# Optimization experiments

Hardware: AMD Instinct MI355X
Metric: run time of the kernel (lower is better)

## Reference

```python
import jax, jax.numpy as jnp
import numpy as np

C_REG = 0.1
MAX_ITER = 15
SIGMA = 0.1  # centering parameter for the interior-point steps


def _qp_solve(G, e, h, A, b, max_iter):
    """Batched primal-dual interior-point solver (fixed iteration count, as QPFunction(maxIter=...)).

    Solves per task: min_z 0.5 z^T G z + e^T z  s.t.  z <= h (inequality matrix is identity),  A z = b.
    G: (t,n,n), e,h: (t,n), A: (t,p,n), b: (t,p). Returns z: (t,n).
    """
    t, n = e.shape
    p = A.shape[1]
    dt = G.dtype
    z = jnp.zeros((t, n), dt)
    s = jnp.ones((t, n), dt)    # slack for z + s = h
    lam = jnp.ones((t, n), dt)  # inequality duals
    nu = jnp.zeros((t, p), dt)  # equality duals
    At = jnp.swapaxes(A, 1, 2)              # (t,n,p)
    eye_n = jnp.eye(n, dtype=dt)
    zeros_pp = jnp.zeros((t, p, p), dt)

    def step(carry, _):
        z, s, lam, nu = carry
        # KKT residuals (infeasible-start Newton)
        rz = jnp.einsum('bij,bj->bi', G, z) + e + lam + jnp.einsum('bpi,bp->bi', A, nu)
        rs = z + s - h
        ra = jnp.einsum('bpi,bi->bp', A, z) - b
        mu = jnp.mean(lam * s, axis=1, keepdims=True)
        # eliminate ds and dlam -> reduced saddle system in (dz, dnu)
        r1 = -rz - (lam * rs - lam * s + SIGMA * mu) / s
        D = lam / s  # diagonal of barrier Hessian contribution
        M_top = jnp.concatenate([G + D[:, :, None] * eye_n, At], axis=2)  # (t,n,n+p)
        M_bot = jnp.concatenate([A, zeros_pp], axis=2)                    # (t,p,n+p)
        M = jnp.concatenate([M_top, M_bot], axis=1)                       # (t,n+p,n+p)
        rhs = jnp.concatenate([r1, -ra], axis=1)
        sol = jnp.linalg.solve(M, rhs[..., None])[..., 0]
        dz, dnu = sol[:, :n], sol[:, n:]
        ds = -rs - dz
        dlam = (lam * dz + lam * rs - lam * s + SIGMA * mu) / s
        # fraction-to-boundary step size keeping s, lam > 0
        ratio_s = jnp.where(ds < 0, -s / ds, jnp.inf)
        ratio_l = jnp.where(dlam < 0, -lam / dlam, jnp.inf)
        alpha = jnp.minimum(1.0, 0.99 * jnp.minimum(ratio_s.min(axis=1), ratio_l.min(axis=1)))[:, None]
        return (z + alpha * dz, s + alpha * ds, lam + alpha * dlam, nu + alpha * dnu), None

    (z, s, lam, nu), _ = jax.lax.scan(step, (z, s, lam, nu), xs=None, length=max_iter)
    return z


def setup_inputs() -> dict:
    key = jax.random.key(0)
    k1, k2, k3 = jax.random.split(key, 3)
    tasks, n_way, n_shot, d = 64, 5, 15, 4096
    n_support = n_way * n_shot          # 75
    n_query = 150
    query = jax.random.normal(k1, (tasks, n_query, d), dtype=jnp.float32)
    support = jax.random.normal(k2, (tasks, n_support, d), dtype=jnp.float32)
    support_labels = jax.random.randint(k3, (tasks, n_support), 0, n_way)
    return {"query": query, "support": support, "support_labels": support_labels,
            "n_way": n_way, "n_shot": n_shot}


def reference(query, support, support_labels, n_way, n_shot):
    t, ns, d = support.shape
    nq = query.shape[1]
    n = ns * n_way
    dt = support.dtype
    # linear kernel Gram matrix on support: (t, ns, ns)
    K = jnp.einsum('bnd,bmd->bnm', support, support)
    # block kernel = K kron I_{n_way}, then + I (the module adds 1.0 * eye)
    I_w = jnp.eye(n_way, dtype=dt)
    block_K = (K[:, :, None, :, None] * I_w[None, None, :, None, :]).reshape(t, n, n)
    G = block_K + jnp.eye(n, dtype=dt)
    # one-hot labels, flattened to (t, ns*n_way)
    y1h = jax.nn.one_hot(support_labels, n_way, dtype=dt).reshape(t, n)
    e = -y1h
    h = C_REG * y1h
    # A = I_{ns} kron ones(1, n_way): sums duals over classes per support point
    A = jnp.tile(jnp.eye(ns, dtype=dt)[:, :, None], (1, 1, n_way)).reshape(ns, n)
    A = jnp.broadcast_to(A, (t, ns, n))
    b = jnp.zeros((t, ns), dt)
    z = _qp_solve(G, e, h, A, b, MAX_ITER)
    qp_sol = z.reshape(t, ns, n_way)
    # compatibility = support . query^T : (t, ns, nq); logits = sum over support
    compat = jnp.einsum('bnd,bqd->bnq', support, query)
    logits = jnp.einsum('bnq,bnw->bqw', compat, qp_sol)  # (t, nq, n_way)
    return logits
```

## Files before the change

kernel.cpp:

```cpp
#include <hip/hip_runtime.h>
#include <math.h>

#define T_TASKS 64
#define NS 75
#define NW 5
#define NTOT 375
#define NQ 150
#define DIM 4096
#define QP_ITERS 15
#define SIGMA 0.1f
#define CREG 0.1f

#define OFF_K   0u
#define OFF_W   369664u
#define OFF_Z   2417664u
#define OFF_S   2441664u
#define OFF_LAM 2465664u
#define OFF_NU  2489664u
#define OFF_TV  2494464u

__global__ void qp_init(float* __restrict__ z, float* __restrict__ s,
                        float* __restrict__ lam, float* __restrict__ nu) {
    int idx = blockIdx.x * 256 + threadIdx.x;
    if (idx < T_TASKS * NTOT) { z[idx] = 0.f; s[idx] = 1.f; lam[idx] = 1.f; }
    if (idx < T_TASKS * NS) nu[idx] = 0.f;
}

__global__ __launch_bounds__(256) void gram_partial(const float* __restrict__ support,
                                                    float* __restrict__ Kp) {
    int qd = blockIdx.x, b = blockIdx.y;
    __shared__ __align__(16) float Ss[80 * 132];
    int tid = threadIdx.x;
    int tx = tid & 15, ty = tid >> 4;
    float acc[5][5];
#pragma unroll
    for (int u = 0; u < 5; u++)
#pragma unroll
        for (int v = 0; v < 5; v++) acc[u][v] = 0.f;
    const float* sb = support + (size_t)b * NS * DIM + qd * 1024;
    for (int cc = 0; cc < 8; cc++) {
        __syncthreads();
        for (int idx = tid; idx < 80 * 32; idx += 256) {
            int r = idx >> 5, d4 = idx & 31;
            float4 v = make_float4(0.f, 0.f, 0.f, 0.f);
            if (r < 75) v = *(const float4*)&sb[(size_t)r * DIM + cc * 128 + d4 * 4];
            *(float4*)&Ss[r * 132 + d4 * 4] = v;
        }
        __syncthreads();
        for (int d4 = 0; d4 < 32; d4++) {
            float4 av[5], bv[5];
#pragma unroll
            for (int u = 0; u < 5; u++) av[u] = *(const float4*)&Ss[(ty * 5 + u) * 132 + d4 * 4];
#pragma unroll
            for (int v = 0; v < 5; v++) bv[v] = *(const float4*)&Ss[(tx * 5 + v) * 132 + d4 * 4];
#pragma unroll
            for (int u = 0; u < 5; u++)
#pragma unroll
                for (int v = 0; v < 5; v++)
                    acc[u][v] += av[u].x * bv[v].x + av[u].y * bv[v].y +
                                 av[u].z * bv[v].z + av[u].w * bv[v].w;
        }
    }
    float* Ko = Kp + (size_t)(qd * 64 + b) * 5776;
#pragma unroll
    for (int u = 0; u < 5; u++) {
        int row = ty * 5 + u;
#pragma unroll
        for (int v = 0; v < 5; v++) {
            int col = tx * 5 + v;
            if (row < 75 && col < 75) Ko[row * 76 + col] = acc[u][v];
        }
    }
}

__global__ void gram_reduce(const float* __restrict__ Kp, float* __restrict__ Kg) {
    int idx = blockIdx.x * 256 + threadIdx.x;
    if (idx >= 64 * 5776) return;
    int rc = idx % 5776;
    int row = rc / 76, col = rc % 76;
    float val;
    if (row < 75 && col < 75)
        val = Kp[idx] + Kp[369664 + idx] + Kp[2 * 369664 + idx] + Kp[3 * 369664 + idx];
    else
        val = (row == col) ? 1.f : 0.f;
    Kg[idx] = val;
}

__device__ __forceinline__ void reg_gj80(float (&M)[5][5],
                                         float (*prow)[80], float (*fcol)[80],
                                         int tx, int ty) {
    for (int k = 0; k < 75; k++) {
        int bf = k & 1;
        if (ty == (k & 15)) {
#pragma unroll
            for (int m = 0; m < 5; m++) {
                if (ty + 16 * m == k) {
#pragma unroll
                    for (int n = 0; n < 5; n++) prow[bf][tx + 16 * n] = M[m][n];
                }
            }
        }
        if (tx == (k & 15)) {
#pragma unroll
            for (int n = 0; n < 5; n++) {
                if (tx + 16 * n == k) {
#pragma unroll
                    for (int m = 0; m < 5; m++) fcol[bf][ty + 16 * m] = M[m][n];
                }
            }
        }
        __syncthreads();
        float pinv = 1.f / prow[bf][k];
        float pv[5], fv[5], ps[5];
#pragma unroll
        for (int n = 0; n < 5; n++) {
            pv[n] = prow[bf][tx + 16 * n];
            ps[n] = pv[n] * pinv;
        }
#pragma unroll
        for (int m = 0; m < 5; m++) {
            int r = ty + 16 * m;
            float f = fcol[bf][r] * pinv;
            fv[m] = (r == k) ? 0.f : f;
        }
#pragma unroll
        for (int m = 0; m < 5; m++) {
            int r = ty + 16 * m;
            bool rk = (r == k);
#pragma unroll
            for (int n = 0; n < 5; n++) {
                int c = tx + 16 * n;
                float val = M[m][n] - fv[m] * pv[n];
                val = rk ? ps[n] : val;
                val = (c == k) ? (rk ? pinv : -fv[m]) : val;
                M[m][n] = val;
            }
        }
    }
}

__global__ __launch_bounds__(256) void factor_kernel(
        const float* __restrict__ Kg, const int* __restrict__ labels,
        const float* __restrict__ zg, const float* __restrict__ sg,
        const float* __restrict__ lamg, const float* __restrict__ nug,
        float* __restrict__ Wg, float* __restrict__ tvg) {
    int w = blockIdx.x, b = blockIdx.y;
    int tid = threadIdx.x;
    int tx = tid & 15, ty = tid >> 4;
    __shared__ float prow[2][80], fcol[2][80];
    __shared__ float zw[80], r1w[80], Dv[80], swv[80], lwv[80], nuwv[80];
    __shared__ int labv[80];
    __shared__ float mred[4];

    float M[5][5];
    const float* Kt = Kg + (size_t)b * 5776;
#pragma unroll
    for (int m = 0; m < 5; m++) {
        int r = ty + 16 * m;
#pragma unroll
        for (int n = 0; n < 5; n++) {
            int c = tx + 16 * n;
            M[m][n] = (r < 76 && c < 76) ? Kt[r * 76 + c] : ((r == c) ? 1.f : 0.f);
        }
    }
    if (tid < 80) {
        float zv = 0.f, sv = 1.f, lv = 0.f, nv = 0.f; int lb = -1;
        if (tid < 75) {
            zv = zg[b * NTOT + tid * NW + w];
            sv = sg[b * NTOT + tid * NW + w];
            lv = lamg[b * NTOT + tid * NW + w];
            nv = nug[b * NS + tid];
            lb = labels[b * NS + tid];
        }
        zw[tid] = zv; swv[tid] = sv; lwv[tid] = lv; nuwv[tid] = nv; labv[tid] = lb;
    }
    float part = 0.f;
    for (int idx = tid; idx < NTOT; idx += 256)
        part += lamg[b * NTOT + idx] * sg[b * NTOT + idx];
#pragma unroll
    for (int off = 32; off > 0; off >>= 1) part += __shfl_xor(part, off, 64);
    if ((tid & 63) == 0) mred[tid >> 6] = part;
    __syncthreads();
    float mu = (mred[0] + mred[1] + mred[2] + mred[3]) * (1.f / (float)NTOT);

    float gp[5];
#pragma unroll
    for (int m = 0; m < 5; m++) {
        float a = 0.f;
#pragma unroll
        for (int n = 0; n < 5; n++) a += M[m][n] * zw[tx + 16 * n];
        gp[m] = a;
    }
#pragma unroll
    for (int off = 1; off < 16; off <<= 1)
#pragma unroll
        for (int m = 0; m < 5; m++) gp[m] += __shfl_xor(gp[m], off, 64);
    if (tx == 0) {
#pragma unroll
        for (int m = 0; m < 5; m++) {
            int r = ty + 16 * m;
            float val = 0.f, dv = 0.f;
            if (r < 75) {
                float sv = swv[r], lv = lwv[r], zv = zw[r];
                float e = (labv[r] == w) ? -1.f : 0.f;
                float h = (labv[r] == w) ? CREG : 0.f;
                float rz = gp[m] + zv + e + lv + nuwv[r];
                float rs = zv + sv - h;
                val = -rz - (lv * rs - lv * sv + SIGMA * mu) / sv;
                dv = lv / sv;
            }
            r1w[r] = val; Dv[r] = dv;
        }
    }
    __syncthreads();
    if (tx == ty) {
#pragma unroll
        for (int m = 0; m < 5; m++) {
            int r = ty + 16 * m;
            if (r < 75) M[m][m] += 1.f + Dv[r];
        }
    }

    reg_gj80(M, prow, fcol, tx, ty);

    float* Wo = Wg + (size_t)(b * NW + w) * 6400;
#pragma unroll
    for (int m = 0; m < 5; m++)
#pragma unroll
        for (int n = 0; n < 5; n++)
            Wo[(m * 5 + n) * 256 + tid] = M[m][n];

    float tp[5];
#pragma unroll
    for (int m = 0; m < 5; m++) {
        float a = 0.f;
#pragma unroll
        for (int n = 0; n < 5; n++) a += M[m][n] * r1w[tx + 16 * n];
        tp[m] = a;
    }
#pragma unroll
    for (int off = 1; off < 16; off <<= 1)
#pragma unroll
        for (int m = 0; m < 5; m++) tp[m] += __shfl_xor(tp[m], off, 64);
    if (tx == 0) {
#pragma unroll
        for (int m = 0; m < 5; m++) {
            int r = ty + 16 * m;
            if (r < 75) tvg[(b * NW + w) * 80 + r] = tp[m];
        }
    }
}

__global__ __launch_bounds__(256) void schur_update_kernel(
        const int* __restrict__ labels,
        float* __restrict__ z, float* __restrict__ s,
        float* __restrict__ lam, float* __restrict__ nu,
        const float* __restrict__ Wg, const float* __restrict__ tvg) {
    int b = blockIdx.x;
    int tid = threadIdx.x;
    int tx = tid & 15, ty = tid >> 4;
    __shared__ float prow[2][80], fcol[2][80];
    __shared__ __align__(16) float rhs[80];
    __shared__ __align__(16) float dnu[80];
    __shared__ float mred[4], ared[4];

    float M[5][5];
    const float* Wb = Wg + (size_t)b * NW * 6400;
#pragma unroll
    for (int m = 0; m < 5; m++)
#pragma unroll
        for (int n = 0; n < 5; n++) {
            float a = 0.f;
#pragma unroll
            for (int ww = 0; ww < 5; ww++)
                a += Wb[ww * 6400 + (m * 5 + n) * 256 + tid];
            M[m][n] = a;
        }
    if (tid < 80) {
        float rv = 0.f;
        if (tid < 75) {
#pragma unroll
            for (int ww = 0; ww < 5; ww++)
                rv += z[b * NTOT + tid * NW + ww] + tvg[(b * NW + ww) * 80 + tid];
        }
        rhs[tid] = rv;
    }
    float part = 0.f;
    for (int idx = tid; idx < NTOT; idx += 256)
        part += lam[b * NTOT + idx] * s[b * NTOT + idx];
#pragma unroll
    for (int off = 32; off > 0; off >>= 1) part += __shfl_xor(part, off, 64);
    if ((tid & 63) == 0) mred[tid >> 6] = part;
    __syncthreads();
    float mu = (mred[0] + mred[1] + mred[2] + mred[3]) * (1.f / (float)NTOT);

    reg_gj80(M, prow, fcol, tx, ty);

    float tp[5];
#pragma unroll
    for (int m = 0; m < 5; m++) {
        float a = 0.f;
#pragma unroll
        for (int n = 0; n < 5; n++) a += M[m][n] * rhs[tx + 16 * n];
        tp[m] = a;
    }
#pragma unroll
    for (int off = 1; off < 16; off <<= 1)
#pragma unroll
        for (int m = 0; m < 5; m++) tp[m] += __shfl_xor(tp[m], off, 64);
    if (tx == 0) {
#pragma unroll
        for (int m = 0; m < 5; m++) dnu[ty + 16 * m] = tp[m];
    }
    __syncthreads();

    float rat = INFINITY;
    float dzv[2], dsv[2], dlv[2], zlv[2], slv[2], llv[2];
#pragma unroll
    for (int pass = 0; pass < 2; pass++) {
        int c = tid + 256 * pass;
        dzv[pass] = 0.f; dsv[pass] = 0.f; dlv[pass] = 0.f;
        zlv[pass] = 0.f; slv[pass] = 1.f; llv[pass] = 0.f;
        if (c < NTOT) {
            int i = c / 5, ww = c - (c / 5) * 5;
            int mi = i >> 4, tyi = i & 15;
            const float* Wr = Wb + ww * 6400 + mi * 5 * 256 + tyi * 16;
            const float4* dn4 = (const float4*)dnu;
            float acc = 0.f;
#pragma unroll
            for (int n = 0; n < 5; n++) {
                const float4* w4 = (const float4*)(Wr + n * 256);
#pragma unroll
                for (int q = 0; q < 4; q++) {
                    float4 x = w4[q], y = dn4[4 * n + q];
                    acc += x.x * y.x + x.y * y.y + x.z * y.z + x.w * y.w;
                }
            }
            float tvl = tvg[(b * NW + ww) * 80 + i];
            float zl = z[b * NTOT + c], sl = s[b * NTOT + c], ll = lam[b * NTOT + c];
            float dz_t = tvl - acc;
            int lb = labels[b * NS + i];
            float h = (lb == ww) ? CREG : 0.f;
            float rs = zl + sl - h;
            float ds_t = -rs - dz_t;
            float dl_t = (ll * dz_t + ll * rs - ll * sl + SIGMA * mu) / sl;
            zlv[pass] = zl; slv[pass] = sl; llv[pass] = ll;
            dzv[pass] = dz_t; dsv[pass] = ds_t; dlv[pass] = dl_t;
            float r1 = (ds_t < 0.f) ? (-sl / ds_t) : INFINITY;
            float r2 = (dl_t < 0.f) ? (-ll / dl_t) : INFINITY;
            rat = fminf(rat, fminf(r1, r2));
        }
    }
#pragma unroll
    for (int off = 32; off > 0; off >>= 1) rat = fminf(rat, __shfl_xor(rat, off, 64));
    if ((tid & 63) == 0) ared[tid >> 6] = rat;
    __syncthreads();
    float alpha = fminf(1.f, 0.99f * fminf(fminf(ared[0], ared[1]), fminf(ared[2], ared[3])));
#pragma unroll
    for (int pass = 0; pass < 2; pass++) {
        int c = tid + 256 * pass;
        if (c < NTOT) {
            z[b * NTOT + c]   = zlv[pass] + alpha * dzv[pass];
            s[b * NTOT + c]   = slv[pass] + alpha * dsv[pass];
            lam[b * NTOT + c] = llv[pass] + alpha * dlv[pass];
        }
    }
    if (tid < 75) nu[b * NS + tid] += alpha * dnu[tid];
}

__global__ __launch_bounds__(256) void v_kernel(const float* __restrict__ support,
                                                const float* __restrict__ z,
                                                float* __restrict__ vbuf) {
    int dc = blockIdx.x, b = blockIdx.y;
    __shared__ float zs[NTOT];
    int tid = threadIdx.x;
    for (int idx = tid; idx < NTOT; idx += 256) zs[idx] = z[b * NTOT + idx];
    __syncthreads();
    int d = dc * 256 + tid;
    float acc[5] = {0.f, 0.f, 0.f, 0.f, 0.f};
    const float* sb = support + (size_t)b * NS * DIM + d;
    for (int ss = 0; ss < NS; ss++) {
        float svv = sb[(size_t)ss * DIM];
#pragma unroll
        for (int w = 0; w < 5; w++) acc[w] += svv * zs[ss * 5 + w];
    }
#pragma unroll
    for (int w = 0; w < 5; w++) vbuf[(size_t)(b * NW + w) * DIM + d] = acc[w];
}

__global__ __launch_bounds__(256) void logits_kernel(const float* __restrict__ query,
                                                     const float* __restrict__ vbuf,
                                                     float* __restrict__ out) {
    int qt = blockIdx.x, b = blockIdx.y;
    __shared__ __align__(16) float vs[5 * 1028];
    int tid = threadIdx.x;
    int lane = tid & 63, wid = tid >> 6;
    float acc[8][5];
#pragma unroll
    for (int r = 0; r < 8; r++)
#pragma unroll
        for (int w = 0; w < 5; w++) acc[r][w] = 0.f;

    for (int c = 0; c < 4; c++) {
        __syncthreads();
        for (int idx = tid; idx < 5120; idx += 256) {
            int w = idx >> 10, dd = idx & 1023;
            vs[w * 1028 + dd] = vbuf[(size_t)(b * NW + w) * DIM + c * 1024 + dd];
        }
        __syncthreads();
#pragma unroll
        for (int ri = 0; ri < 8; ri++) {
            int r = wid + ri * 4;
            if (r < 30) {
                int q = qt * 30 + r;
                const float* qp = query + (size_t)(b * NQ + q) * DIM + c * 1024;
#pragma unroll
                for (int j = 0; j < 4; j++) {
                    int d = lane * 4 + j * 256;
                    float4 qv = *(const float4*)(qp + d);
#pragma unroll
                    for (int w = 0; w < 5; w++) {
                        float4 vv = *(const float4*)(&vs[w * 1028 + d]);
                        acc[ri][w] += qv.x * vv.x + qv.y * vv.y + qv.z * vv.z + qv.w * vv.w;
                    }
                }
            }
        }
    }
#pragma unroll
    for (int ri = 0; ri < 8; ri++) {
        int r = wid + ri * 4;
#pragma unroll
        for (int w = 0; w < 5; w++) {
            float v = acc[ri][w];
            for (int off = 32; off > 0; off >>= 1) v += __shfl_xor(v, off, 64);
            if (r < 30 && lane == 0)
                out[(size_t)(b * NQ + qt * 30 + r) * NW + w] = v;
        }
    }
}

extern "C" void kernel_launch(void* const* d_in, const int* in_sizes, int n_in,
                              void* d_out, int out_size, void* d_ws, size_t ws_size,
                              hipStream_t stream) {
    const float* query   = (const float*)d_in[0];
    const float* support = (const float*)d_in[1];
    const int*   labels  = (const int*)d_in[2];
    float* out = (float*)d_out;
    float* ws  = (float*)d_ws;

    float* Kg   = ws + OFF_K;
    float* Wg   = ws + OFF_W;
    float* Kp   = ws + OFF_W;
    float* vbuf = ws + OFF_W;
    float* z    = ws + OFF_Z;
    float* s    = ws + OFF_S;
    float* lam  = ws + OFF_LAM;
    float* nu   = ws + OFF_NU;
    float* tv   = ws + OFF_TV;

    qp_init<<<(T_TASKS * NTOT + 255) / 256, 256, 0, stream>>>(z, s, lam, nu);
    gram_partial<<<dim3(4, T_TASKS), 256, 0, stream>>>(support, Kp);
    gram_reduce<<<(64 * 5776 + 255) / 256, 256, 0, stream>>>(Kp, Kg);
    for (int it = 0; it < QP_ITERS; it++) {
        factor_kernel<<<dim3(NW, T_TASKS), 256, 0, stream>>>(Kg, labels, z, s, lam, nu, Wg, tv);
        schur_update_kernel<<<T_TASKS, 256, 0, stream>>>(labels, z, s, lam, nu, Wg, tv);
    }
    v_kernel<<<dim3(16, T_TASKS), 256, 0, stream>>>(support, z, vbuf);
    logits_kernel<<<dim3(5, T_TASKS), 256, 0, stream>>>(query, vbuf, out);
}
```

Before: 2.167 ms.

## Fuse all QP iterations into one persistent per-task kernel with register-resident inverses

Replaces the 30 per-iteration launches (factor and Schur update) with a single kernel per task that keeps z, s, lambda and nu in shared memory and holds all five class-block inverses in registers across all 15 iterations. This removes global round-trips of the W matrices and the launch overhead. The Gram kernel is also split 8 ways with double-buffered prefetch and stores only the lower triangle. In exchange, only 64 blocks run during the QP phase and register pressure is high (launch_bounds 256,1), so occupancy and possible spilling are the risks.

```diff
diff --git a/kernel.cpp b/kernel.cpp
--- a/kernel.cpp
+++ b/kernel.cpp
@@ -14,22 +14,12 @@
 #define OFF_K   0u
 #define OFF_W   369664u
 #define OFF_Z   2417664u
-#define OFF_S   2441664u
-#define OFF_LAM 2465664u
-#define OFF_NU  2489664u
-#define OFF_TV  2494464u
-
-__global__ void qp_init(float* __restrict__ z, float* __restrict__ s,
-                        float* __restrict__ lam, float* __restrict__ nu) {
-    int idx = blockIdx.x * 256 + threadIdx.x;
-    if (idx < T_TASKS * NTOT) { z[idx] = 0.f; s[idx] = 1.f; lam[idx] = 1.f; }
-    if (idx < T_TASKS * NS) nu[idx] = 0.f;
-}
-
-__global__ __launch_bounds__(256) void gram_partial(const float* __restrict__ support,
-                                                    float* __restrict__ Kp) {
-    int qd = blockIdx.x, b = blockIdx.y;
-    __shared__ __align__(16) float Ss[80 * 132];
+#define TRI_SZ  2850
+
+__global__ __launch_bounds__(256) void gram8(const float* __restrict__ support,
+                                             float* __restrict__ Kp) {
+    int p = blockIdx.x, b = blockIdx.y;
+    __shared__ __align__(16) float Ss[2][80][68];
     int tid = threadIdx.x;
     int tx = tid & 15, ty = tid >> 4;
     float acc[5][5];
@@ -37,22 +27,39 @@
     for (int u = 0; u < 5; u++)
 #pragma unroll
         for (int v = 0; v < 5; v++) acc[u][v] = 0.f;
-    const float* sb = support + (size_t)b * NS * DIM + qd * 1024;
-    for (int cc = 0; cc < 8; cc++) {
-        __syncthreads();
-        for (int idx = tid; idx < 80 * 32; idx += 256) {
-            int r = idx >> 5, d4 = idx & 31;
-            float4 v = make_float4(0.f, 0.f, 0.f, 0.f);
-            if (r < 75) v = *(const float4*)&sb[(size_t)r * DIM + cc * 128 + d4 * 4];
-            *(float4*)&Ss[r * 132 + d4 * 4] = v;
-        }
-        __syncthreads();
-        for (int d4 = 0; d4 < 32; d4++) {
+    const float* sb = support + (size_t)b * NS * DIM + p * 512;
+
+    float4 pf[5];
+#define G8_ISSUE(c)                                                        \
+    {                                                                      \
+        _Pragma("unroll")                                                  \
+        for (int j = 0; j < 5; j++) {                                      \
+            int idx = tid + 256 * j;                                       \
+            int r = idx >> 4, q = idx & 15;                                \
+            pf[j] = (r < 75) ? *(const float4*)&sb[(size_t)r * DIM + (c) * 64 + q * 4] \
+                             : make_float4(0.f, 0.f, 0.f, 0.f);            \
+        }                                                                  \
+    }
+#define G8_COMMIT(c)                                                       \
+    {                                                                      \
+        _Pragma("unroll")                                                  \
+        for (int j = 0; j < 5; j++) {                                      \
+            int idx = tid + 256 * j;                                       \
+            int r = idx >> 4, q = idx & 15;                                \
+            *(float4*)&Ss[(c) & 1][r][q * 4] = pf[j];                      \
+        }                                                                  \
+    }
+    G8_ISSUE(0);
+    G8_COMMIT(0);
+    for (int c = 0; c < 8; c++) {
+        if (c < 7) G8_ISSUE(c + 1);
+        __syncthreads();
+        for (int d4 = 0; d4 < 16; d4++) {
             float4 av[5], bv[5];
 #pragma unroll
-            for (int u = 0; u < 5; u++) av[u] = *(const float4*)&Ss[(ty * 5 + u) * 132 + d4 * 4];
-#pragma unroll
-            for (int v = 0; v < 5; v++) bv[v] = *(const float4*)&Ss[(tx * 5 + v) * 132 + d4 * 4];
+            for (int u = 0; u < 5; u++) av[u] = *(const float4*)&Ss[c & 1][ty * 5 + u][d4 * 4];
+#pragma unroll
+            for (int v = 0; v < 5; v++) bv[v] = *(const float4*)&Ss[c & 1][tx * 5 + v][d4 * 4];
 #pragma unroll
             for (int u = 0; u < 5; u++)
 #pragma unroll
@@ -60,329 +67,355 @@
                     acc[u][v] += av[u].x * bv[v].x + av[u].y * bv[v].y +
                                  av[u].z * bv[v].z + av[u].w * bv[v].w;
         }
-    }
-    float* Ko = Kp + (size_t)(qd * 64 + b) * 5776;
+        if (c < 7) G8_COMMIT(c + 1);
+    }
+    float* Ko = Kp + (size_t)(p * 64 + b) * TRI_SZ;
 #pragma unroll
     for (int u = 0; u < 5; u++) {
         int row = ty * 5 + u;
 #pragma unroll
         for (int v = 0; v < 5; v++) {
             int col = tx * 5 + v;
-            if (row < 75 && col < 75) Ko[row * 76 + col] = acc[u][v];
+            if (row < 75 && col < 75 && row >= col)
+                Ko[row * (row + 1) / 2 + col] = acc[u][v];
         }
     }
 }
 
 __global__ void gram_reduce(const float* __restrict__ Kp, float* __restrict__ Kg) {
     int idx = blockIdx.x * 256 + threadIdx.x;
-    if (idx >= 64 * 5776) return;
-    int rc = idx % 5776;
+    if (idx >= T_TASKS * 5776) return;
+    int b = idx / 5776, rc = idx % 5776;
     int row = rc / 76, col = rc % 76;
     float val;
-    if (row < 75 && col < 75)
-        val = Kp[idx] + Kp[369664 + idx] + Kp[2 * 369664 + idx] + Kp[3 * 369664 + idx];
-    else
+    if (row < 75 && col < 75) {
+        int i = row > col ? row : col, j = row > col ? col : row;
+        int t = i * (i + 1) / 2 + j;
+        val = 0.f;
+#pragma unroll
+        for (int p = 0; p < 8; p++)
+            val += Kp[(size_t)(p * 64 + b) * TRI_SZ + t];
+    } else {
         val = (row == col) ? 1.f : 0.f;
+    }
     Kg[idx] = val;
 }
 
-__device__ __forceinline__ void reg_gj80(float (&M)[5][5],
-                                         float (*prow)[80], float (*fcol)[80],
-                                         int tx, int ty) {
+template <int NM>
+__device__ __forceinline__ void reg_gj_multi(float (&M)[NM][5][5],
+                                             float (*prow)[2][80],
+                                             float (*fcol)[2][80],
+                                             int tx, int ty) {
     for (int k = 0; k < 75; k++) {
         int bf = k & 1;
-        if (ty == (k & 15)) {
-#pragma unroll
-            for (int m = 0; m < 5; m++) {
+        int km = k & 15, kd = k >> 4;
+        if (ty == km) {
+#pragma unroll
+            for (int m = 0; m < 5; m++)
                 if (ty + 16 * m == k) {
 #pragma unroll
-                    for (int n = 0; n < 5; n++) prow[bf][tx + 16 * n] = M[m][n];
-                }
-            }
-        }
-        if (tx == (k & 15)) {
-#pragma unroll
-            for (int n = 0; n < 5; n++) {
+                    for (int w = 0; w < NM; w++)
+#pragma unroll
+                        for (int n = 0; n < 5; n++)
+                            prow[w][bf][tx + 16 * n] = M[w][m][n];
+                }
+        }
+        if (tx == km) {
+#pragma unroll
+            for (int n = 0; n < 5; n++)
                 if (tx + 16 * n == k) {
 #pragma unroll
-                    for (int m = 0; m < 5; m++) fcol[bf][ty + 16 * m] = M[m][n];
-                }
-            }
-        }
-        __syncthreads();
-        float pinv = 1.f / prow[bf][k];
-        float pv[5], fv[5], ps[5];
-#pragma unroll
-        for (int n = 0; n < 5; n++) {
-            pv[n] = prow[bf][tx + 16 * n];
-            ps[n] = pv[n] * pinv;
-        }
-#pragma unroll
-        for (int m = 0; m < 5; m++) {
-            int r = ty + 16 * m;
-            float f = fcol[bf][r] * pinv;
-            fv[m] = (r == k) ? 0.f : f;
-        }
-#pragma unroll
-        for (int m = 0; m < 5; m++) {
-            int r = ty + 16 * m;
-            bool rk = (r == k);
+                    for (int w = 0; w < NM; w++)
+#pragma unroll
+                        for (int m = 0; m < 5; m++)
+                            fcol[w][bf][ty + 16 * m] = M[w][m][n];
+                }
+        }
+        __syncthreads();
+        if (tx == km) {
+#pragma unroll
+            for (int n = 0; n < 5; n++)
+                if (n == kd) {
+#pragma unroll
+                    for (int w = 0; w < NM; w++)
+#pragma unroll
+                        for (int m = 0; m < 5; m++)
+                            M[w][m][n] = (ty + 16 * m == k) ? 1.f : 0.f;
+                }
+        }
+#pragma unroll
+        for (int w = 0; w < NM; w++) {
+            float pinv = 1.f / prow[w][bf][k];
+            float pv2[5], fv2[5];
 #pragma unroll
             for (int n = 0; n < 5; n++) {
                 int c = tx + 16 * n;
-                float val = M[m][n] - fv[m] * pv[n];
-                val = rk ? ps[n] : val;
-                val = (c == k) ? (rk ? pinv : -fv[m]) : val;
-                M[m][n] = val;
-            }
-        }
-    }
-}
-
-__global__ __launch_bounds__(256) void factor_kernel(
+                float pp = prow[w][bf][c];
+                pv2[n] = (c == k) ? 1.f : pp;
+            }
+#pragma unroll
+            for (int m = 0; m < 5; m++) {
+                int r = ty + 16 * m;
+                float f = fcol[w][bf][r] * pinv;
+                fv2[m] = (r == k) ? (1.f - pinv) : f;
+            }
+#pragma unroll
+            for (int m = 0; m < 5; m++)
+#pragma unroll
+                for (int n = 0; n < 5; n++)
+                    M[w][m][n] -= fv2[m] * pv2[n];
+        }
+    }
+}
+
+__global__ __launch_bounds__(256, 1) void qp_solve(
         const float* __restrict__ Kg, const int* __restrict__ labels,
-        const float* __restrict__ zg, const float* __restrict__ sg,
-        const float* __restrict__ lamg, const float* __restrict__ nug,
-        float* __restrict__ Wg, float* __restrict__ tvg) {
-    int w = blockIdx.x, b = blockIdx.y;
-    int tid = threadIdx.x;
-    int tx = tid & 15, ty = tid >> 4;
-    __shared__ float prow[2][80], fcol[2][80];
-    __shared__ float zw[80], r1w[80], Dv[80], swv[80], lwv[80], nuwv[80];
-    __shared__ int labv[80];
-    __shared__ float mred[4];
-
-    float M[5][5];
-    const float* Kt = Kg + (size_t)b * 5776;
-#pragma unroll
-    for (int m = 0; m < 5; m++) {
-        int r = ty + 16 * m;
-#pragma unroll
-        for (int n = 0; n < 5; n++) {
-            int c = tx + 16 * n;
-            M[m][n] = (r < 76 && c < 76) ? Kt[r * 76 + c] : ((r == c) ? 1.f : 0.f);
-        }
-    }
-    if (tid < 80) {
-        float zv = 0.f, sv = 1.f, lv = 0.f, nv = 0.f; int lb = -1;
-        if (tid < 75) {
-            zv = zg[b * NTOT + tid * NW + w];
-            sv = sg[b * NTOT + tid * NW + w];
-            lv = lamg[b * NTOT + tid * NW + w];
-            nv = nug[b * NS + tid];
-            lb = labels[b * NS + tid];
-        }
-        zw[tid] = zv; swv[tid] = sv; lwv[tid] = lv; nuwv[tid] = nv; labv[tid] = lb;
-    }
-    float part = 0.f;
-    for (int idx = tid; idx < NTOT; idx += 256)
-        part += lamg[b * NTOT + idx] * sg[b * NTOT + idx];
-#pragma unroll
-    for (int off = 32; off > 0; off >>= 1) part += __shfl_xor(part, off, 64);
-    if ((tid & 63) == 0) mred[tid >> 6] = part;
-    __syncthreads();
-    float mu = (mred[0] + mred[1] + mred[2] + mred[3]) * (1.f / (float)NTOT);
-
-    float gp[5];
-#pragma unroll
-    for (int m = 0; m < 5; m++) {
-        float a = 0.f;
-#pragma unroll
-        for (int n = 0; n < 5; n++) a += M[m][n] * zw[tx + 16 * n];
-        gp[m] = a;
-    }
-#pragma unroll
-    for (int off = 1; off < 16; off <<= 1)
-#pragma unroll
-        for (int m = 0; m < 5; m++) gp[m] += __shfl_xor(gp[m], off, 64);
-    if (tx == 0) {
-#pragma unroll
-        for (int m = 0; m < 5; m++) {
-            int r = ty + 16 * m;
-            float val = 0.f, dv = 0.f;
-            if (r < 75) {
-                float sv = swv[r], lv = lwv[r], zv = zw[r];
-                float e = (labv[r] == w) ? -1.f : 0.f;
-                float h = (labv[r] == w) ? CREG : 0.f;
-                float rz = gp[m] + zv + e + lv + nuwv[r];
-                float rs = zv + sv - h;
-                val = -rz - (lv * rs - lv * sv + SIGMA * mu) / sv;
-                dv = lv / sv;
-            }
-            r1w[r] = val; Dv[r] = dv;
-        }
-    }
-    __syncthreads();
-    if (tx == ty) {
-#pragma unroll
-        for (int m = 0; m < 5; m++) {
-            int r = ty + 16 * m;
-            if (r < 75) M[m][m] += 1.f + Dv[r];
-        }
-    }
-
-    reg_gj80(M, prow, fcol, tx, ty);
-
-    float* Wo = Wg + (size_t)(b * NW + w) * 6400;
-#pragma unroll
-    for (int m = 0; m < 5; m++)
-#pragma unroll
-        for (int n = 0; n < 5; n++)
-            Wo[(m * 5 + n) * 256 + tid] = M[m][n];
-
-    float tp[5];
-#pragma unroll
-    for (int m = 0; m < 5; m++) {
-        float a = 0.f;
-#pragma unroll
-        for (int n = 0; n < 5; n++) a += M[m][n] * r1w[tx + 16 * n];
-        tp[m] = a;
-    }
-#pragma unroll
-    for (int off = 1; off < 16; off <<= 1)
-#pragma unroll
-        for (int m = 0; m < 5; m++) tp[m] += __shfl_xor(tp[m], off, 64);
-    if (tx == 0) {
-#pragma unroll
-        for (int m = 0; m < 5; m++) {
-            int r = ty + 16 * m;
-            if (r < 75) tvg[(b * NW + w) * 80 + r] = tp[m];
-        }
-    }
-}
-
-__global__ __launch_bounds__(256) void schur_update_kernel(
-        const int* __restrict__ labels,
-        float* __restrict__ z, float* __restrict__ s,
-        float* __restrict__ lam, float* __restrict__ nu,
-        const float* __restrict__ Wg, const float* __restrict__ tvg) {
+        float* __restrict__ zout) {
     int b = blockIdx.x;
     int tid = threadIdx.x;
     int tx = tid & 15, ty = tid >> 4;
-    __shared__ float prow[2][80], fcol[2][80];
-    __shared__ __align__(16) float rhs[80];
-    __shared__ __align__(16) float dnu[80];
-    __shared__ float mred[4], ared[4];
-
-    float M[5][5];
-    const float* Wb = Wg + (size_t)b * NW * 6400;
-#pragma unroll
-    for (int m = 0; m < 5; m++)
+
+    __shared__ float prow[5][2][80], fcol[5][2][80];
+    __shared__ float zs[400], ss[400], ls[400];
+    __shared__ float nus[80];
+    __shared__ int labv[80];
+    __shared__ float r1w[5][80], Dv[5][80], tvs[5][80], dzs[5][80];
+    __shared__ float rhs[80], dnu[80], mred[4], ared[4];
+
+    float Kreg[5][5];
+    const float* Kt = Kg + (size_t)b * 5776;
+#pragma unroll
+    for (int m = 0; m < 5; m++) {
+        int r = ty + 16 * m;
 #pragma unroll
         for (int n = 0; n < 5; n++) {
-            float a = 0.f;
-#pragma unroll
-            for (int ww = 0; ww < 5; ww++)
-                a += Wb[ww * 6400 + (m * 5 + n) * 256 + tid];
-            M[m][n] = a;
-        }
+            int c = tx + 16 * n;
+            Kreg[m][n] = (r < 76 && c < 76) ? Kt[r * 76 + c] : ((r == c) ? 1.f : 0.f);
+        }
+    }
+    for (int idx = tid; idx < 400; idx += 256) {
+        zs[idx] = 0.f;
+        ss[idx] = (idx < NTOT) ? 1.f : 0.f;
+        ls[idx] = (idx < NTOT) ? 1.f : 0.f;
+    }
     if (tid < 80) {
-        float rv = 0.f;
-        if (tid < 75) {
-#pragma unroll
-            for (int ww = 0; ww < 5; ww++)
-                rv += z[b * NTOT + tid * NW + ww] + tvg[(b * NW + ww) * 80 + tid];
-        }
-        rhs[tid] = rv;
-    }
-    float part = 0.f;
-    for (int idx = tid; idx < NTOT; idx += 256)
-        part += lam[b * NTOT + idx] * s[b * NTOT + idx];
-#pragma unroll
-    for (int off = 32; off > 0; off >>= 1) part += __shfl_xor(part, off, 64);
-    if ((tid & 63) == 0) mred[tid >> 6] = part;
+        nus[tid] = 0.f;
+        labv[tid] = (tid < 75) ? labels[b * NS + tid] : -1;
+    }
     __syncthreads();
-    float mu = (mred[0] + mred[1] + mred[2] + mred[3]) * (1.f / (float)NTOT);
-
-    reg_gj80(M, prow, fcol, tx, ty);
-
-    float tp[5];
-#pragma unroll
-    for (int m = 0; m < 5; m++) {
-        float a = 0.f;
-#pragma unroll
-        for (int n = 0; n < 5; n++) a += M[m][n] * rhs[tx + 16 * n];
-        tp[m] = a;
-    }
-#pragma unroll
-    for (int off = 1; off < 16; off <<= 1)
-#pragma unroll
-        for (int m = 0; m < 5; m++) tp[m] += __shfl_xor(tp[m], off, 64);
-    if (tx == 0) {
-#pragma unroll
-        for (int m = 0; m < 5; m++) dnu[ty + 16 * m] = tp[m];
-    }
-    __syncthreads();
-
-    float rat = INFINITY;
-    float dzv[2], dsv[2], dlv[2], zlv[2], slv[2], llv[2];
-#pragma unroll
-    for (int pass = 0; pass < 2; pass++) {
-        int c = tid + 256 * pass;
-        dzv[pass] = 0.f; dsv[pass] = 0.f; dlv[pass] = 0.f;
-        zlv[pass] = 0.f; slv[pass] = 1.f; llv[pass] = 0.f;
-        if (c < NTOT) {
-            int i = c / 5, ww = c - (c / 5) * 5;
-            int mi = i >> 4, tyi = i & 15;
-            const float* Wr = Wb + ww * 6400 + mi * 5 * 256 + tyi * 16;
-            const float4* dn4 = (const float4*)dnu;
-            float acc = 0.f;
+
+    float MW[5][5][5];
+    float S[1][5][5];
+
+    for (int it = 0; it < QP_ITERS; it++) {
+        {
+            float part = 0.f;
+            for (int idx = tid; idx < NTOT; idx += 256) part += ls[idx] * ss[idx];
+#pragma unroll
+            for (int off = 32; off > 0; off >>= 1) part += __shfl_xor(part, off, 64);
+            if ((tid & 63) == 0) mred[tid >> 6] = part;
+        }
+        __syncthreads();
+        float mu = (mred[0] + mred[1] + mred[2] + mred[3]) * (1.f / (float)NTOT);
+
+#pragma unroll
+        for (int w = 0; w < 5; w++) {
+            float gp[5];
+#pragma unroll
+            for (int m = 0; m < 5; m++) {
+                float a = 0.f;
+#pragma unroll
+                for (int n = 0; n < 5; n++) a += Kreg[m][n] * zs[(tx + 16 * n) * 5 + w];
+                gp[m] = a;
+            }
+#pragma unroll
+            for (int off = 1; off < 16; off <<= 1)
+#pragma unroll
+                for (int m = 0; m < 5; m++) gp[m] += __shfl_xor(gp[m], off, 64);
+            if (tx == 0) {
+#pragma unroll
+                for (int m = 0; m < 5; m++) {
+                    int r = ty + 16 * m;
+                    float val = 0.f, dv = 0.f;
+                    if (r < 75) {
+                        float sv = ss[r * 5 + w], lv = ls[r * 5 + w], zv = zs[r * 5 + w];
+                        float e = (labv[r] == w) ? -1.f : 0.f;
+                        float h = (labv[r] == w) ? CREG : 0.f;
+                        float rz = gp[m] + zv + e + lv + nus[r];
+                        float rs = zv + sv - h;
+                        val = -rz - (lv * rs - lv * sv + SIGMA * mu) / sv;
+                        dv = lv / sv;
+                    }
+                    r1w[w][r] = val;
+                    Dv[w][r] = dv;
+                }
+            }
+        }
+        __syncthreads();
+
+#pragma unroll
+        for (int w = 0; w < 5; w++) {
+            float dval[5];
+#pragma unroll
+            for (int m = 0; m < 5; m++) dval[m] = Dv[w][ty + 16 * m];
+#pragma unroll
+            for (int m = 0; m < 5; m++) {
+                int r = ty + 16 * m;
+#pragma unroll
+                for (int n = 0; n < 5; n++) {
+                    float v = Kreg[m][n];
+                    if (m == n && tx == ty && r < 75) v += 1.f + dval[m];
+                    MW[w][m][n] = v;
+                }
+            }
+        }
+
+        reg_gj_multi<5>(MW, prow, fcol, tx, ty);
+
+#pragma unroll
+        for (int w = 0; w < 5; w++) {
+            float tp[5];
+#pragma unroll
+            for (int m = 0; m < 5; m++) {
+                float a = 0.f;
+#pragma unroll
+                for (int n = 0; n < 5; n++) a += MW[w][m][n] * r1w[w][tx + 16 * n];
+                tp[m] = a;
+            }
+#pragma unroll
+            for (int off = 1; off < 16; off <<= 1)
+#pragma unroll
+                for (int m = 0; m < 5; m++) tp[m] += __shfl_xor(tp[m], off, 64);
+            if (tx == 0) {
+#pragma unroll
+                for (int m = 0; m < 5; m++) tvs[w][ty + 16 * m] = tp[m];
+            }
+        }
+        __syncthreads();
+
+#pragma unroll
+        for (int m = 0; m < 5; m++)
 #pragma unroll
             for (int n = 0; n < 5; n++) {
-                const float4* w4 = (const float4*)(Wr + n * 256);
-#pragma unroll
-                for (int q = 0; q < 4; q++) {
-                    float4 x = w4[q], y = dn4[4 * n + q];
-                    acc += x.x * y.x + x.y * y.y + x.z * y.z + x.w * y.w;
-                }
-            }
-            float tvl = tvg[(b * NW + ww) * 80 + i];
-            float zl = z[b * NTOT + c], sl = s[b * NTOT + c], ll = lam[b * NTOT + c];
-            float dz_t = tvl - acc;
-            int lb = labels[b * NS + i];
-            float h = (lb == ww) ? CREG : 0.f;
-            float rs = zl + sl - h;
-            float ds_t = -rs - dz_t;
-            float dl_t = (ll * dz_t + ll * rs - ll * sl + SIGMA * mu) / sl;
-            zlv[pass] = zl; slv[pass] = sl; llv[pass] = ll;
-            dzv[pass] = dz_t; dsv[pass] = ds_t; dlv[pass] = dl_t;
-            float r1 = (ds_t < 0.f) ? (-sl / ds_t) : INFINITY;
-            float r2 = (dl_t < 0.f) ? (-ll / dl_t) : INFINITY;
-            rat = fminf(rat, fminf(r1, r2));
-        }
-    }
-#pragma unroll
-    for (int off = 32; off > 0; off >>= 1) rat = fminf(rat, __shfl_xor(rat, off, 64));
-    if ((tid & 63) == 0) ared[tid >> 6] = rat;
-    __syncthreads();
-    float alpha = fminf(1.f, 0.99f * fminf(fminf(ared[0], ared[1]), fminf(ared[2], ared[3])));
-#pragma unroll
-    for (int pass = 0; pass < 2; pass++) {
-        int c = tid + 256 * pass;
-        if (c < NTOT) {
-            z[b * NTOT + c]   = zlv[pass] + alpha * dzv[pass];
-            s[b * NTOT + c]   = slv[pass] + alpha * dsv[pass];
-            lam[b * NTOT + c] = llv[pass] + alpha * dlv[pass];
-        }
-    }
-    if (tid < 75) nu[b * NS + tid] += alpha * dnu[tid];
+                float a = MW[0][m][n];
+#pragma unroll
+                for (int w = 1; w < 5; w++) a += MW[w][m][n];
+                S[0][m][n] = a;
+            }
+        if (tid < 80) {
+            float rv = 0.f;
+            if (tid < 75) {
+#pragma unroll
+                for (int w = 0; w < 5; w++) rv += zs[tid * 5 + w] + tvs[w][tid];
+            }
+            rhs[tid] = rv;
+        }
+        __syncthreads();
+
+        reg_gj_multi<1>(S, prow, fcol, tx, ty);
+
+        {
+            float tp[5];
+#pragma unroll
+            for (int m = 0; m < 5; m++) {
+                float a = 0.f;
+#pragma unroll
+                for (int n = 0; n < 5; n++) a += S[0][m][n] * rhs[tx + 16 * n];
+                tp[m] = a;
+            }
+#pragma unroll
+            for (int off = 1; off < 16; off <<= 1)
+#pragma unroll
+                for (int m = 0; m < 5; m++) tp[m] += __shfl_xor(tp[m], off, 64);
+            if (tx == 0) {
+#pragma unroll
+                for (int m = 0; m < 5; m++) dnu[ty + 16 * m] = tp[m];
+            }
+        }
+        __syncthreads();
+
+#pragma unroll
+        for (int w = 0; w < 5; w++) {
+            float tp[5];
+#pragma unroll
+            for (int m = 0; m < 5; m++) {
+                float a = 0.f;
+#pragma unroll
+                for (int n = 0; n < 5; n++) a += MW[w][m][n] * dnu[tx + 16 * n];
+                tp[m] = a;
+            }
+#pragma unroll
+            for (int off = 1; off < 16; off <<= 1)
+#pragma unroll
+                for (int m = 0; m < 5; m++) tp[m] += __shfl_xor(tp[m], off, 64);
+            if (tx == 0) {
+#pragma unroll
+                for (int m = 0; m < 5; m++) {
+                    int r = ty + 16 * m;
+                    dzs[w][r] = tvs[w][r] - tp[m];
+                }
+            }
+        }
+        __syncthreads();
+
+        float rat = INFINITY;
+        float dzv[2], dsv[2], dlv[2], zlv[2], slv[2], llv[2];
+#pragma unroll
+        for (int pass = 0; pass < 2; pass++) {
+            int c = tid + 256 * pass;
+            dzv[pass] = 0.f; dsv[pass] = 0.f; dlv[pass] = 0.f;
+            zlv[pass] = 0.f; slv[pass] = 1.f; llv[pass] = 0.f;
+            if (c < NTOT) {
+                int i = c / 5, w = c - (c / 5) * 5;
+                float dz_t = dzs[w][i];
+                float zl = zs[c], sl = ss[c], ll = ls[c];
+                float h = (labv[i] == w) ? CREG : 0.f;
+                float rs = zl + sl - h;
+                float ds_t = -rs - dz_t;
+                float dl_t = (ll * dz_t + ll * rs - ll * sl + SIGMA * mu) / sl;
+                zlv[pass] = zl; slv[pass] = sl; llv[pass] = ll;
+                dzv[pass] = dz_t; dsv[pass] = ds_t; dlv[pass] = dl_t;
+                float rr1 = (ds_t < 0.f) ? (-sl / ds_t) : INFINITY;
+                float rr2 = (dl_t < 0.f) ? (-ll / dl_t) : INFINITY;
+                rat = fminf(rat, fminf(rr1, rr2));
+            }
+        }
+#pragma unroll
+        for (int off = 32; off > 0; off >>= 1) rat = fminf(rat, __shfl_xor(rat, off, 64));
+        if ((tid & 63) == 0) ared[tid >> 6] = rat;
+        __syncthreads();
+        float alpha = fminf(1.f, 0.99f * fminf(fminf(ared[0], ared[1]), fminf(ared[2], ared[3])));
+#pragma unroll
+        for (int pass = 0; pass < 2; pass++) {
+            int c = tid + 256 * pass;
+            if (c < NTOT) {
+                zs[c] = zlv[pass] + alpha * dzv[pass];
+                ss[c] = slv[pass] + alpha * dsv[pass];
+                ls[c] = llv[pass] + alpha * dlv[pass];
+            }
+        }
+        if (tid < 75) nus[tid] += alpha * dnu[tid];
+        __syncthreads();
+    }
+
+    for (int idx = tid; idx < NTOT; idx += 256) zout[b * NTOT + idx] = zs[idx];
 }
 
 __global__ __launch_bounds__(256) void v_kernel(const float* __restrict__ support,
                                                 const float* __restrict__ z,
                                                 float* __restrict__ vbuf) {
     int dc = blockIdx.x, b = blockIdx.y;
-    __shared__ float zs[NTOT];
+    __shared__ float zsm[NTOT];
     int tid = threadIdx.x;
-    for (int idx = tid; idx < NTOT; idx += 256) zs[idx] = z[b * NTOT + idx];
+    for (int idx = tid; idx < NTOT; idx += 256) zsm[idx] = z[b * NTOT + idx];
     __syncthreads();
     int d = dc * 256 + tid;
     float acc[5] = {0.f, 0.f, 0.f, 0.f, 0.f};
     const float* sb = support + (size_t)b * NS * DIM + d;
-    for (int ss = 0; ss < NS; ss++) {
-        float svv = sb[(size_t)ss * DIM];
-#pragma unroll
-        for (int w = 0; w < 5; w++) acc[w] += svv * zs[ss * 5 + w];
+    for (int ssi = 0; ssi < NS; ssi++) {
+        float svv = sb[(size_t)ssi * DIM];
+#pragma unroll
+        for (int w = 0; w < 5; w++) acc[w] += svv * zsm[ssi * 5 + w];
     }
 #pragma unroll
     for (int w = 0; w < 5; w++) vbuf[(size_t)(b * NW + w) * DIM + d] = acc[w];
@@ -450,22 +483,13 @@
     float* ws  = (float*)d_ws;
 
     float* Kg   = ws + OFF_K;
-    float* Wg   = ws + OFF_W;
     float* Kp   = ws + OFF_W;
     float* vbuf = ws + OFF_W;
     float* z    = ws + OFF_Z;
-    float* s    = ws + OFF_S;
-    float* lam  = ws + OFF_LAM;
-    float* nu   = ws + OFF_NU;
-    float* tv   = ws + OFF_TV;
-
-    qp_init<<<(T_TASKS * NTOT + 255) / 256, 256, 0, stream>>>(z, s, lam, nu);
-    gram_partial<<<dim3(4, T_TASKS), 256, 0, stream>>>(support, Kp);
-    gram_reduce<<<(64 * 5776 + 255) / 256, 256, 0, stream>>>(Kp, Kg);
-    for (int it = 0; it < QP_ITERS; it++) {
-        factor_kernel<<<dim3(NW, T_TASKS), 256, 0, stream>>>(Kg, labels, z, s, lam, nu, Wg, tv);
-        schur_update_kernel<<<T_TASKS, 256, 0, stream>>>(labels, z, s, lam, nu, Wg, tv);
-    }
+
+    gram8<<<dim3(8, T_TASKS), 256, 0, stream>>>(support, Kp);
+    gram_reduce<<<(T_TASKS * 5776 + 255) / 256, 256, 0, stream>>>(Kp, Kg);
+    qp_solve<<<T_TASKS, 256, 0, stream>>>(Kg, labels, z);
     v_kernel<<<dim3(16, T_TASKS), 256, 0, stream>>>(support, z, vbuf);
     logits_kernel<<<dim3(5, T_TASKS), 256, 0, stream>>>(query, vbuf, out);
 }
```

Result: slower. 3.073 ms (+41.8%).
